# Kernel optimization log

Hardware: AMD Instinct MI355X
Metric: run time of the kernel (lower is better)

The kernel has to match this reference:

```python
import jax, jax.numpy as jnp
import numpy as np

B, H, S, E = 16384, 16, 1, 64
N_OTHERS = 4


def setup_inputs() -> dict:
    key = jax.random.key(0)
    ks = jax.random.split(key, N_OTHERS + 2)
    inp = {f"others_{i}": jax.random.normal(ks[i], (B, H, S, E), dtype=jnp.float32)
           for i in range(N_OTHERS)}
    inp["main"] = jax.random.normal(ks[N_OTHERS], (B, H, S, E), dtype=jnp.float32)
    inp["W"] = jax.random.normal(ks[N_OTHERS + 1], (E, E), dtype=jnp.float32) * (1.0 / np.sqrt(E))
    return inp


def reference(others_0, others_1, others_2, others_3, main, W):
    # mean over the 'others' modalities: (B, H, 1, E)
    mean = (others_0 + others_1 + others_2 + others_3) / 4.0
    m = jnp.squeeze(mean, 2)        # (B, H, E)
    main_sq = jnp.squeeze(main, 2)  # (B, H, E)
    # bilinear score: mean @ W @ main^T -> (B, H, H)
    score = jnp.einsum('bhe,ef,bgf->bhg', m, W, main_sq)
    attn = jax.nn.softmax(score, axis=-1)      # (B, H, H)
    context = jnp.einsum('bhg,bge->bhe', attn, main_sq)  # (B, H, E)
    return context, attn
```

## Files before the change

### kernel.cpp

```cpp
#include <hip/hip_runtime.h>

#define NBATCH 16384
#define H 16
#define E 64
#define NB 4
#define NWAVE 4
#define NBLK (NBATCH / (NB * NWAVE))

typedef __attribute__((ext_vector_type(8))) short short8v;
typedef __attribute__((ext_vector_type(4))) float f32x4;

#define LGKM0 do { asm volatile("s_waitcnt lgkmcnt(0)" ::: "memory"); \
                   __builtin_amdgcn_sched_barrier(0); } while (0)

__global__ __launch_bounds__(256, 3) void ovo_kernel(
    const float* __restrict__ o0, const float* __restrict__ o1,
    const float* __restrict__ o2, const float* __restrict__ o3,
    const float* __restrict__ mn, const float* __restrict__ W,
    float* __restrict__ ctx_out, float* __restrict__ attn_out)
{
    __shared__ __align__(16) unsigned short sWfrag[4][2][2][512];
    __shared__ float sT[NWAVE][2][H * 68];

    const int tid = threadIdx.x;
    const int l   = tid & 63;
    const int wv  = tid >> 6;

    for (int r = 0; r < 16; ++r) {
        const int flat = r * 256 + tid;
        const float w = W[flat];
        const int e = flat >> 6, f = flat & 63;
        const int t = f >> 4, col = f & 15;
        const int s = e >> 5, khi = (e >> 3) & 3, i = e & 7;
        const unsigned int wb = __float_as_uint(w);
        const unsigned int hb = wb & 0xFFFF0000u;
        const float lof = w - __uint_as_float(hb);
        const unsigned int lb = __float_as_uint(lof);
        const int L = col + 16 * khi;
        sWfrag[t][s][0][L * 8 + i] = (unsigned short)(hb >> 16);
        sWfrag[t][s][1][L * 8 + i] = (unsigned short)(lb >> 16);
    }
    __syncthreads();

    float* const sU    = &sT[wv][0][0];
    float* const sMain = &sT[wv][1][0];

    const int q = l >> 4;
    const int c = l & 15;

#pragma unroll 1
    for (int it = 0; it < NB; ++it) {
        const int batch = it * (NBLK * NWAVE) + blockIdx.x * NWAVE + wv;
        const size_t base = (size_t)batch * (H * E);

        float4 mo[2][2];
#pragma unroll
        for (int s = 0; s < 2; ++s)
#pragma unroll
            for (int c01 = 0; c01 < 2; ++c01) {
                const size_t off = base + c * 64 + 32 * s + 8 * q + 4 * c01;
                float4 a = *(const float4*)(o0 + off);
                float4 b = *(const float4*)(o1 + off);
                float4 g = *(const float4*)(o2 + off);
                float4 d = *(const float4*)(o3 + off);
                mo[s][c01].x = (a.x + b.x) + (g.x + d.x);
                mo[s][c01].y = (a.y + b.y) + (g.y + d.y);
                mo[s][c01].z = (a.z + b.z) + (g.z + d.z);
                mo[s][c01].w = (a.w + b.w) + (g.w + d.w);
            }
        float4 rv[4];
#pragma unroll
        for (int k = 0; k < 4; ++k)
            rv[k] = *(const float4*)(mn + base + k * 256 + l * 4);

#pragma unroll
        for (int k = 0; k < 4; ++k) {
            const int flat = k * 256 + l * 4;
            *(float4*)&sMain[(flat >> 6) * 68 + (flat & 63)] = rv[k];
        }

        short8v ahi[2], alo[2];
#pragma unroll
        for (int s = 0; s < 2; ++s) {
            float ms[8];
            ms[0] = mo[s][0].x; ms[1] = mo[s][0].y; ms[2] = mo[s][0].z; ms[3] = mo[s][0].w;
            ms[4] = mo[s][1].x; ms[5] = mo[s][1].y; ms[6] = mo[s][1].z; ms[7] = mo[s][1].w;
#pragma unroll
            for (int i = 0; i < 8; ++i) {
                const float m = ms[i] * 0.25f;
                const unsigned int mb = __float_as_uint(m);
                const unsigned int hb = mb & 0xFFFF0000u;
                const float lof = m - __uint_as_float(hb);
                ahi[s][i] = (short)(hb >> 16);
                alo[s][i] = (short)(__float_as_uint(lof) >> 16);
            }
        }

#pragma unroll
        for (int t = 0; t < 4; ++t) {
            short8v bh0 = *(const short8v*)&sWfrag[t][0][0][l * 8];
            short8v bl0 = *(const short8v*)&sWfrag[t][0][1][l * 8];
            short8v bh1 = *(const short8v*)&sWfrag[t][1][0][l * 8];
            short8v bl1 = *(const short8v*)&sWfrag[t][1][1][l * 8];
            f32x4 acc = {0.f, 0.f, 0.f, 0.f};
            acc = __builtin_amdgcn_mfma_f32_16x16x32_bf16(ahi[0], bh0, acc, 0, 0, 0);
            acc = __builtin_amdgcn_mfma_f32_16x16x32_bf16(alo[0], bh0, acc, 0, 0, 0);
            acc = __builtin_amdgcn_mfma_f32_16x16x32_bf16(ahi[0], bl0, acc, 0, 0, 0);
            acc = __builtin_amdgcn_mfma_f32_16x16x32_bf16(ahi[1], bh1, acc, 0, 0, 0);
            acc = __builtin_amdgcn_mfma_f32_16x16x32_bf16(alo[1], bh1, acc, 0, 0, 0);
            acc = __builtin_amdgcn_mfma_f32_16x16x32_bf16(ahi[1], bl1, acc, 0, 0, 0);
#pragma unroll
            for (int j = 0; j < 4; ++j)
                sU[(4 * q + j) * 68 + 16 * t + c] = acc[j];
        }
        LGKM0;

        const int hp = l >> 2, gp = l & 3;
        const int g0 = gp * 4;
        float scr[4] = {0.f, 0.f, 0.f, 0.f};
#pragma unroll
        for (int f0 = 0; f0 < 64; f0 += 4) {
            float4 a0 = *(const float4*)&sU[hp * 68 + f0];
            const float* pa = (const float*)&a0;
            float4 b[4];
#pragma unroll
            for (int j = 0; j < 4; ++j)
                b[j] = *(const float4*)&sMain[(g0 + j) * 68 + f0];
#pragma unroll
            for (int j = 0; j < 4; ++j) {
                const float* pb = (const float*)&b[j];
#pragma unroll
                for (int u = 0; u < 4; ++u)
                    scr[j] = fmaf(pa[u], pb[u], scr[j]);
            }
        }

        {
            float mx = fmaxf(fmaxf(scr[0], scr[1]), fmaxf(scr[2], scr[3]));
            mx = fmaxf(mx, __shfl_xor(mx, 1));
            mx = fmaxf(mx, __shfl_xor(mx, 2));
            float e0 = __expf(scr[0] - mx), e1 = __expf(scr[1] - mx);
            float e2 = __expf(scr[2] - mx), e3 = __expf(scr[3] - mx);
            float sum = (e0 + e1) + (e2 + e3);
            sum += __shfl_xor(sum, 1);
            sum += __shfl_xor(sum, 2);
            const float inv = 1.0f / sum;
            float4 a4 = make_float4(e0 * inv, e1 * inv, e2 * inv, e3 * inv);
            *(float4*)(attn_out + (size_t)batch * (H * H) + l * 4) = a4;
            const float* pa4 = (const float*)&a4;
#pragma unroll
            for (int j = 0; j < 4; ++j)
                sU[(g0 + j) * 20 + hp] = pa4[j];
        }
        LGKM0;

        {
            const int ht = q, et = c;
            const int h0 = ht * 4, e0c = et * 4;
            f32x4 acc2[4] = {{0.f,0.f,0.f,0.f},{0.f,0.f,0.f,0.f},
                             {0.f,0.f,0.f,0.f},{0.f,0.f,0.f,0.f}};
#pragma unroll
            for (int g = 0; g < 16; ++g) {
                float4 bv = *(const float4*)&sMain[g * 68 + e0c];
                float4 av = *(const float4*)&sU[g * 20 + h0];
                const float* pb = (const float*)&bv;
                const float* pa = (const float*)&av;
#pragma unroll
                for (int i = 0; i < 4; ++i)
#pragma unroll
                    for (int j = 0; j < 4; ++j)
                        acc2[i][j] = fmaf(pa[i], pb[j], acc2[i][j]);
            }
            float* cp = ctx_out + base;
#pragma unroll
            for (int i = 0; i < 4; ++i)
                *(float4*)(cp + (h0 + i) * 64 + e0c) =
                    make_float4(acc2[i][0], acc2[i][1], acc2[i][2], acc2[i][3]);
        }
    }
}

extern "C" void kernel_launch(void* const* d_in, const int* in_sizes, int n_in,
                              void* d_out, int out_size, void* d_ws, size_t ws_size,
                              hipStream_t stream) {
    const float* o0 = (const float*)d_in[0];
    const float* o1 = (const float*)d_in[1];
    const float* o2 = (const float*)d_in[2];
    const float* o3 = (const float*)d_in[3];
    const float* mn = (const float*)d_in[4];
    const float* W  = (const float*)d_in[5];
    float* ctx  = (float*)d_out;
    float* attn = ctx + (size_t)NBATCH * H * E;
    hipLaunchKernelGGL(ovo_kernel, dim3(NBLK), dim3(NWAVE * 64), 0, stream,
                       o0, o1, o2, o3, mn, W, ctx, attn);
}
```

Measured before the change: 88.59 us.

## Prefetch next batch's others inputs and compute scores with split-bf16 MFMA

Loads the four 'others' tiles for the next batch into registers while the current batch is being processed, starting with a prologue load before the W staging. The score computation U·main^T moves from scalar FMAs to three-term split-bf16 MFMAs, and the softmax becomes a per-column shuffle reduction. The explicit lgkmcnt waits are replaced by plain compiler fences. This hides global load latency and cuts VALU work, at the cost of more registers, a possible occupancy drop, and scattered scalar attn stores. Removing the explicit waits between LDS writes and reads within a wave may depend on compiler-inserted waitcnt for correctness.

```diff
diff --git a/kernel.cpp b/kernel.cpp
--- a/kernel.cpp
+++ b/kernel.cpp
@@ -10,8 +10,17 @@
 typedef __attribute__((ext_vector_type(8))) short short8v;
 typedef __attribute__((ext_vector_type(4))) float f32x4;
 
-#define LGKM0 do { asm volatile("s_waitcnt lgkmcnt(0)" ::: "memory"); \
-                   __builtin_amdgcn_sched_barrier(0); } while (0)
+#define CFENCE asm volatile("" ::: "memory")
+
+__device__ __forceinline__ void bf16split8(const float* v, short8v& hi, short8v& lo) {
+#pragma unroll
+    for (int i = 0; i < 8; ++i) {
+        const unsigned int b = __float_as_uint(v[i]);
+        const unsigned int hb = b & 0xFFFF0000u;
+        hi[i] = (short)(hb >> 16);
+        lo[i] = (short)(__float_as_uint(v[i] - __uint_as_float(hb)) >> 16);
+    }
+}
 
 __global__ __launch_bounds__(256, 3) void ovo_kernel(
     const float* __restrict__ o0, const float* __restrict__ o1,
@@ -25,9 +34,25 @@
     const int tid = threadIdx.x;
     const int l   = tid & 63;
     const int wv  = tid >> 6;
-
-    for (int r = 0; r < 16; ++r) {
-        const int flat = r * 256 + tid;
+    const int r   = l & 15;
+    const int q   = l >> 4;
+
+    float4 po0[4], po1[4], po2[4], po3[4];
+    {
+        const size_t base = (size_t)(blockIdx.x * NWAVE + wv) * (H * E);
+#pragma unroll
+        for (int sc = 0; sc < 4; ++sc) {
+            const int s = sc >> 1, c01 = sc & 1;
+            const size_t off = base + r * 64 + 32 * s + 8 * q + 4 * c01;
+            po0[sc] = *(const float4*)(o0 + off);
+            po1[sc] = *(const float4*)(o1 + off);
+            po2[sc] = *(const float4*)(o2 + off);
+            po3[sc] = *(const float4*)(o3 + off);
+        }
+    }
+
+    for (int rr = 0; rr < 16; ++rr) {
+        const int flat = rr * 256 + tid;
         const float w = W[flat];
         const int e = flat >> 6, f = flat & 63;
         const int t = f >> 4, col = f & 15;
@@ -35,66 +60,53 @@
         const unsigned int wb = __float_as_uint(w);
         const unsigned int hb = wb & 0xFFFF0000u;
         const float lof = w - __uint_as_float(hb);
-        const unsigned int lb = __float_as_uint(lof);
         const int L = col + 16 * khi;
         sWfrag[t][s][0][L * 8 + i] = (unsigned short)(hb >> 16);
-        sWfrag[t][s][1][L * 8 + i] = (unsigned short)(lb >> 16);
+        sWfrag[t][s][1][L * 8 + i] = (unsigned short)(__float_as_uint(lof) >> 16);
     }
     __syncthreads();
 
     float* const sU    = &sT[wv][0][0];
     float* const sMain = &sT[wv][1][0];
-
-    const int q = l >> 4;
-    const int c = l & 15;
 
 #pragma unroll 1
     for (int it = 0; it < NB; ++it) {
         const int batch = it * (NBLK * NWAVE) + blockIdx.x * NWAVE + wv;
         const size_t base = (size_t)batch * (H * E);
 
-        float4 mo[2][2];
-#pragma unroll
-        for (int s = 0; s < 2; ++s)
-#pragma unroll
-            for (int c01 = 0; c01 < 2; ++c01) {
-                const size_t off = base + c * 64 + 32 * s + 8 * q + 4 * c01;
-                float4 a = *(const float4*)(o0 + off);
-                float4 b = *(const float4*)(o1 + off);
-                float4 g = *(const float4*)(o2 + off);
-                float4 d = *(const float4*)(o3 + off);
-                mo[s][c01].x = (a.x + b.x) + (g.x + d.x);
-                mo[s][c01].y = (a.y + b.y) + (g.y + d.y);
-                mo[s][c01].z = (a.z + b.z) + (g.z + d.z);
-                mo[s][c01].w = (a.w + b.w) + (g.w + d.w);
-            }
-        float4 rv[4];
-#pragma unroll
-        for (int k = 0; k < 4; ++k)
-            rv[k] = *(const float4*)(mn + base + k * 256 + l * 4);
-
-#pragma unroll
-        for (int k = 0; k < 4; ++k) {
-            const int flat = k * 256 + l * 4;
-            *(float4*)&sMain[(flat >> 6) * 68 + (flat & 63)] = rv[k];
-        }
-
         short8v ahi[2], alo[2];
 #pragma unroll
         for (int s = 0; s < 2; ++s) {
             float ms[8];
-            ms[0] = mo[s][0].x; ms[1] = mo[s][0].y; ms[2] = mo[s][0].z; ms[3] = mo[s][0].w;
-            ms[4] = mo[s][1].x; ms[5] = mo[s][1].y; ms[6] = mo[s][1].z; ms[7] = mo[s][1].w;
-#pragma unroll
-            for (int i = 0; i < 8; ++i) {
-                const float m = ms[i] * 0.25f;
-                const unsigned int mb = __float_as_uint(m);
-                const unsigned int hb = mb & 0xFFFF0000u;
-                const float lof = m - __uint_as_float(hb);
-                ahi[s][i] = (short)(hb >> 16);
-                alo[s][i] = (short)(__float_as_uint(lof) >> 16);
+#pragma unroll
+            for (int c01 = 0; c01 < 2; ++c01) {
+                const int sc = s * 2 + c01;
+                ms[c01 * 4 + 0] = ((po0[sc].x + po1[sc].x) + (po2[sc].x + po3[sc].x)) * 0.25f;
+                ms[c01 * 4 + 1] = ((po0[sc].y + po1[sc].y) + (po2[sc].y + po3[sc].y)) * 0.25f;
+                ms[c01 * 4 + 2] = ((po0[sc].z + po1[sc].z) + (po2[sc].z + po3[sc].z)) * 0.25f;
+                ms[c01 * 4 + 3] = ((po0[sc].w + po1[sc].w) + (po2[sc].w + po3[sc].w)) * 0.25f;
             }
-        }
+            bf16split8(ms, ahi[s], alo[s]);
+        }
+
+        float4 pm[4];
+#pragma unroll
+        for (int k = 0; k < 4; ++k)
+            pm[k] = *(const float4*)(mn + base + k * 256 + l * 4);
+
+        if (it + 1 < NB) {
+            const size_t nbase = base + (size_t)(NBLK * NWAVE) * (H * E);
+#pragma unroll
+            for (int sc = 0; sc < 4; ++sc) {
+                const int s = sc >> 1, c01 = sc & 1;
+                const size_t off = nbase + r * 64 + 32 * s + 8 * q + 4 * c01;
+                po0[sc] = *(const float4*)(o0 + off);
+                po1[sc] = *(const float4*)(o1 + off);
+                po2[sc] = *(const float4*)(o2 + off);
+                po3[sc] = *(const float4*)(o3 + off);
+            }
+        }
+        CFENCE;
 
 #pragma unroll
         for (int t = 0; t < 4; ++t) {
@@ -111,60 +123,66 @@
             acc = __builtin_amdgcn_mfma_f32_16x16x32_bf16(ahi[1], bl1, acc, 0, 0, 0);
 #pragma unroll
             for (int j = 0; j < 4; ++j)
-                sU[(4 * q + j) * 68 + 16 * t + c] = acc[j];
-        }
-        LGKM0;
-
-        const int hp = l >> 2, gp = l & 3;
-        const int g0 = gp * 4;
-        float scr[4] = {0.f, 0.f, 0.f, 0.f};
-#pragma unroll
-        for (int f0 = 0; f0 < 64; f0 += 4) {
-            float4 a0 = *(const float4*)&sU[hp * 68 + f0];
-            const float* pa = (const float*)&a0;
-            float4 b[4];
-#pragma unroll
-            for (int j = 0; j < 4; ++j)
-                b[j] = *(const float4*)&sMain[(g0 + j) * 68 + f0];
-#pragma unroll
-            for (int j = 0; j < 4; ++j) {
-                const float* pb = (const float*)&b[j];
-#pragma unroll
-                for (int u = 0; u < 4; ++u)
-                    scr[j] = fmaf(pa[u], pb[u], scr[j]);
-            }
-        }
-
-        {
-            float mx = fmaxf(fmaxf(scr[0], scr[1]), fmaxf(scr[2], scr[3]));
+                sU[(4 * q + j) * 68 + 16 * t + r] = acc[j];
+        }
+        CFENCE;
+
+#pragma unroll
+        for (int k = 0; k < 4; ++k) {
+            const int flat = k * 256 + l * 4;
+            *(float4*)&sMain[(flat >> 6) * 68 + (flat & 63)] = pm[k];
+        }
+        CFENCE;
+
+        f32x4 d3 = {0.f, 0.f, 0.f, 0.f};
+#pragma unroll
+        for (int ks = 0; ks < 2; ++ks) {
+            float av[8], bv[8];
+            *(float4*)&av[0] = *(const float4*)&sU[r * 68 + ks * 32 + 8 * q];
+            *(float4*)&av[4] = *(const float4*)&sU[r * 68 + ks * 32 + 8 * q + 4];
+            *(float4*)&bv[0] = *(const float4*)&sMain[r * 68 + ks * 32 + 8 * q];
+            *(float4*)&bv[4] = *(const float4*)&sMain[r * 68 + ks * 32 + 8 * q + 4];
+            short8v ah, al2, bh, bl;
+            bf16split8(av, ah, al2);
+            bf16split8(bv, bh, bl);
+            d3 = __builtin_amdgcn_mfma_f32_16x16x32_bf16(ah,  bh, d3, 0, 0, 0);
+            d3 = __builtin_amdgcn_mfma_f32_16x16x32_bf16(al2, bh, d3, 0, 0, 0);
+            d3 = __builtin_amdgcn_mfma_f32_16x16x32_bf16(ah,  bl, d3, 0, 0, 0);
+        }
+        CFENCE;
+
+        float at4[4];
+#pragma unroll
+        for (int j = 0; j < 4; ++j) {
+            float mx = d3[j];
             mx = fmaxf(mx, __shfl_xor(mx, 1));
             mx = fmaxf(mx, __shfl_xor(mx, 2));
-            float e0 = __expf(scr[0] - mx), e1 = __expf(scr[1] - mx);
-            float e2 = __expf(scr[2] - mx), e3 = __expf(scr[3] - mx);
-            float sum = (e0 + e1) + (e2 + e3);
-            sum += __shfl_xor(sum, 1);
-            sum += __shfl_xor(sum, 2);
-            const float inv = 1.0f / sum;
-            float4 a4 = make_float4(e0 * inv, e1 * inv, e2 * inv, e3 * inv);
-            *(float4*)(attn_out + (size_t)batch * (H * H) + l * 4) = a4;
-            const float* pa4 = (const float*)&a4;
-#pragma unroll
-            for (int j = 0; j < 4; ++j)
-                sU[(g0 + j) * 20 + hp] = pa4[j];
-        }
-        LGKM0;
+            mx = fmaxf(mx, __shfl_xor(mx, 4));
+            mx = fmaxf(mx, __shfl_xor(mx, 8));
+            const float e = __expf(d3[j] - mx);
+            float sm = e;
+            sm += __shfl_xor(sm, 1);
+            sm += __shfl_xor(sm, 2);
+            sm += __shfl_xor(sm, 4);
+            sm += __shfl_xor(sm, 8);
+            at4[j] = e * __builtin_amdgcn_rcpf(sm);
+        }
+        *(float4*)&sU[r * 20 + 4 * q] = make_float4(at4[0], at4[1], at4[2], at4[3]);
+#pragma unroll
+        for (int j = 0; j < 4; ++j)
+            attn_out[(size_t)batch * (H * H) + (4 * q + j) * 16 + r] = at4[j];
+        CFENCE;
 
         {
-            const int ht = q, et = c;
-            const int h0 = ht * 4, e0c = et * 4;
+            const int h0 = q * 4, e0c = r * 4;
             f32x4 acc2[4] = {{0.f,0.f,0.f,0.f},{0.f,0.f,0.f,0.f},
                              {0.f,0.f,0.f,0.f},{0.f,0.f,0.f,0.f}};
 #pragma unroll
             for (int g = 0; g < 16; ++g) {
-                float4 bv = *(const float4*)&sMain[g * 68 + e0c];
-                float4 av = *(const float4*)&sU[g * 20 + h0];
-                const float* pb = (const float*)&bv;
-                const float* pa = (const float*)&av;
+                float4 bvv = *(const float4*)&sMain[g * 68 + e0c];
+                float4 avv = *(const float4*)&sU[g * 20 + h0];
+                const float* pb = (const float*)&bvv;
+                const float* pa = (const float*)&avv;
 #pragma unroll
                 for (int i = 0; i < 4; ++i)
 #pragma unroll
@@ -177,6 +195,7 @@
                 *(float4*)(cp + (h0 + i) * 64 + e0c) =
                     make_float4(acc2[i][0], acc2[i][1], acc2[i][2], acc2[i][3]);
         }
+        CFENCE;
     }
 }
 
```

New measurement: 137.9 us. +55.6%, slower.
